# Kernel optimization log

Hardware: AMD Instinct MI355X
Metric: run time of the kernel (lower is better)

Reference implementation:

```python
import jax, jax.numpy as jnp
import numpy as np

# e2m1 FP4 positive magnitudes {0,0.5,1,1.5,2,3,4,6}/6, normalized to [0,1]
FP4_LEVELS = jnp.array([0.0, 1.0/12, 1.0/6, 1.0/4, 1.0/3, 1.0/2, 2.0/3, 1.0], dtype=jnp.float32)


def create_affp_numbers(max_val, min_val, percentile):
    # max_val, min_val: (R, G) per-group extrema -> (R, G, 16) asymmetric-float codebook
    pos = (max_val * percentile)[..., None] * FP4_LEVELS  # (R, G, 8)
    neg = (min_val * percentile)[..., None] * FP4_LEVELS  # (R, G, 8)
    return jnp.concatenate([neg, pos], axis=-1)            # (R, G, 16)


def setup_inputs() -> dict:
    key = jax.random.key(0)
    x = jax.random.normal(key, (4096, 4096), dtype=jnp.float32)
    return {"x": x, "group_size": 128, "percentile": 1}


def reference(x, group_size, percentile):
    R, C = x.shape
    G = C // group_size
    xg = x.reshape(R, G, group_size)                      # grouped view (split along dim=1)
    mx = jnp.max(xg, axis=-1)                             # (R, G)
    mn = jnp.min(xg, axis=-1)                             # (R, G)
    code = create_affp_numbers(mx, mn, jnp.float32(percentile))  # (R, G, 16)
    # full broadcast distances, argmin, gather (as in the torch source)
    dist = jnp.abs(xg[..., None] - code[:, :, None, :])   # (R, G, gs, 16)
    idx = jnp.argmin(dist, axis=-1)                       # (R, G, gs)
    q = jnp.take_along_axis(code, idx, axis=-1)           # (R, G, gs)
    return q.reshape(R, C)
```

## Files before the change

### kernel.cpp

```cpp
#include <hip/hip_runtime.h>


typedef float vfloat4 __attribute__((ext_vector_type(4)));

template <int CTRL>
__device__ __forceinline__ float dpp_mov_f32(float v) {
    return __int_as_float(__builtin_amdgcn_update_dpp(
        0, __float_as_int(v), CTRL, 0xF, 0xF, true));
}

__device__ __forceinline__ float swz_xor16_f32(float v) {
    return __int_as_float(__builtin_amdgcn_ds_swizzle(__float_as_int(v), 0x401F));
}

__global__ __launch_bounds__(256) void quant_af4_kernel(
    const float* __restrict__ x,
    const int* __restrict__ pctl_ptr,
    float* __restrict__ out,
    int n)
{
    const float LEV1 = (float)(1.0 / 12.0);
    const float LEV2 = (float)(1.0 / 6.0);
    const float LEV3 = (float)(1.0 / 4.0);
    const float LEV4 = (float)(1.0 / 3.0);
    const float LEV5 = (float)(1.0 / 2.0);
    const float LEV6 = (float)(2.0 / 3.0);
    const float LEV7 = 1.0f;

    const float percentile = (float)(*pctl_ptr);

    const int tid = blockIdx.x * blockDim.x + threadIdx.x;
    const long long base = (long long)tid * 4;
    if (base >= n) return;

    const vfloat4 v = *reinterpret_cast<const vfloat4*>(x + base);
    float vv[4] = {v.x, v.y, v.z, v.w};

    float mx = fmaxf(fmaxf(vv[0], vv[1]), fmaxf(vv[2], vv[3]));
    float mn = fminf(fminf(vv[0], vv[1]), fminf(vv[2], vv[3]));

    mx = fmaxf(mx, swz_xor16_f32(mx));
    mn = fminf(mn, swz_xor16_f32(mn));
    mx = fmaxf(mx, dpp_mov_f32<0xB1>(mx));
    mn = fminf(mn, dpp_mov_f32<0xB1>(mn));
    mx = fmaxf(mx, dpp_mov_f32<0x4E>(mx));
    mn = fminf(mn, dpp_mov_f32<0x4E>(mn));
    mx = fmaxf(mx, dpp_mov_f32<0x141>(mx));
    mn = fminf(mn, dpp_mov_f32<0x141>(mn));
    mx = fmaxf(mx, dpp_mov_f32<0x140>(mx));
    mn = fminf(mn, dpp_mov_f32<0x140>(mn));

    const float smx  = mx * percentile;
    const float smn  = mn * percentile;
    const float nabs = -smn;

    float r[4];

    if (smn <= 0.0f && smx >= 0.0f) {
        #pragma unroll
        for (int e = 0; e < 4; ++e) {
            const float xv = vv[e];
            const float a  = fabsf(xv);
            const float sp = (xv > 0.0f) ? smx : nabs;
            float dprev = a;
            float bv    = 0.0f;
            #pragma unroll
            for (int k = 1; k < 8; ++k) {
                const float L = (k == 1) ? LEV1 : (k == 2) ? LEV2 : (k == 3) ? LEV3
                              : (k == 4) ? LEV4 : (k == 5) ? LEV5 : (k == 6) ? LEV6
                              : LEV7;
                const float c = sp * L;
                const float d = a - c;
                if (fabsf(d) < fabsf(dprev)) bv = c;
                dprev = d;
            }
            const unsigned sb = __float_as_uint(xv) & 0x80000000u;
            r[e] = __uint_as_float(__float_as_uint(bv) | sb);
        }
    } else {
        float code[16];
        code[0]  = smn * 0.0f; code[1]  = smn * LEV1; code[2]  = smn * LEV2;
        code[3]  = smn * LEV3; code[4]  = smn * LEV4; code[5]  = smn * LEV5;
        code[6]  = smn * LEV6; code[7]  = smn * LEV7;
        code[8]  = smx * 0.0f; code[9]  = smx * LEV1; code[10] = smx * LEV2;
        code[11] = smx * LEV3; code[12] = smx * LEV4; code[13] = smx * LEV5;
        code[14] = smx * LEV6; code[15] = smx * LEV7;
        #pragma unroll
        for (int e = 0; e < 4; ++e) {
            const float xv = vv[e];
            float bd = fabsf(xv - code[0]);
            float bv = code[0];
            #pragma unroll
            for (int k = 1; k < 16; ++k) {
                const float d = fabsf(xv - code[k]);
                if (d < bd) { bd = d; bv = code[k]; }
            }
            r[e] = bv;
        }
    }

    vfloat4 q = {r[0], r[1], r[2], r[3]};
    __builtin_nontemporal_store(q, reinterpret_cast<vfloat4*>(out + base));
}

extern "C" void kernel_launch(void* const* d_in, const int* in_sizes, int n_in,
                              void* d_out, int out_size, void* d_ws, size_t ws_size,
                              hipStream_t stream) {
    const float* x    = (const float*)d_in[0];
    const int*   pctl = (const int*)d_in[2];
    float*       out  = (float*)d_out;

    const int n = out_size;
    const int threads = 256;
    const int elems_per_block = threads * 4;
    const int blocks = (n + elems_per_block - 1) / elems_per_block;

    quant_af4_kernel<<<blocks, threads, 0, stream>>>(x, pctl, out, n);
}
```

Baseline: 25.22 us.

## Use persistent grid-stride warps with software-prefetched next segment loads

Replaces the one-thread-per-float4 launch with a capped grid of 2048 blocks whose wavefronts loop over 256-element segments. Each wavefront loads the next segment before quantizing the current one, so memory latency overlaps with compute and block launch overhead drops. This costs extra registers for the prefetched vector and fewer resident waves. It assumes n is a multiple of 256, which holds for this group layout.

Result: slower. 27.26 us (+8.1%).

```diff
diff --git a/kernel.cpp b/kernel.cpp
--- a/kernel.cpp
+++ b/kernel.cpp
@@ -13,12 +13,7 @@
     return __int_as_float(__builtin_amdgcn_ds_swizzle(__float_as_int(v), 0x401F));
 }
 
-__global__ __launch_bounds__(256) void quant_af4_kernel(
-    const float* __restrict__ x,
-    const int* __restrict__ pctl_ptr,
-    float* __restrict__ out,
-    int n)
-{
+__device__ __forceinline__ vfloat4 quantize_seg(vfloat4 v, float percentile) {
     const float LEV1 = (float)(1.0 / 12.0);
     const float LEV2 = (float)(1.0 / 6.0);
     const float LEV3 = (float)(1.0 / 4.0);
@@ -27,18 +22,10 @@
     const float LEV6 = (float)(2.0 / 3.0);
     const float LEV7 = 1.0f;
 
-    const float percentile = (float)(*pctl_ptr);
-
-    const int tid = blockIdx.x * blockDim.x + threadIdx.x;
-    const long long base = (long long)tid * 4;
-    if (base >= n) return;
-
-    const vfloat4 v = *reinterpret_cast<const vfloat4*>(x + base);
     float vv[4] = {v.x, v.y, v.z, v.w};
 
     float mx = fmaxf(fmaxf(vv[0], vv[1]), fmaxf(vv[2], vv[3]));
     float mn = fminf(fminf(vv[0], vv[1]), fminf(vv[2], vv[3]));
-
     mx = fmaxf(mx, swz_xor16_f32(mx));
     mn = fminf(mn, swz_xor16_f32(mn));
     mx = fmaxf(mx, dpp_mov_f32<0xB1>(mx));
@@ -100,7 +87,46 @@
     }
 
     vfloat4 q = {r[0], r[1], r[2], r[3]};
-    __builtin_nontemporal_store(q, reinterpret_cast<vfloat4*>(out + base));
+    return q;
+}
+
+__global__ __launch_bounds__(256) void quant_af4_kernel(
+    const float* __restrict__ x,
+    const int* __restrict__ pctl_ptr,
+    float* __restrict__ out,
+    int n)
+{
+    const float percentile = (float)(*pctl_ptr);
+
+    const int lane = threadIdx.x & 63;
+    const int wpb  = blockDim.x >> 6;
+    const int wid  = blockIdx.x * wpb + (threadIdx.x >> 6);
+    const int nw   = gridDim.x * wpb;
+    const int nseg = n >> 8;
+
+    int seg = wid;
+    if (seg >= nseg) return;
+
+    long long base = (long long)seg * 256 + lane * 4;
+    vfloat4 v = *reinterpret_cast<const vfloat4*>(x + base);
+
+    for (;;) {
+        const int nextseg = seg + nw;
+        const bool have_next = (nextseg < nseg);
+        vfloat4 vn;
+        if (have_next) {
+            vn = *reinterpret_cast<const vfloat4*>(
+                     x + (long long)nextseg * 256 + lane * 4);
+        }
+
+        const vfloat4 q = quantize_seg(v, percentile);
+        __builtin_nontemporal_store(q, reinterpret_cast<vfloat4*>(out + base));
+
+        if (!have_next) break;
+        seg  = nextseg;
+        base = (long long)seg * 256 + lane * 4;
+        v    = vn;
+    }
 }
 
 extern "C" void kernel_launch(void* const* d_in, const int* in_sizes, int n_in,
@@ -112,8 +138,10 @@
 
     const int n = out_size;
     const int threads = 256;
-    const int elems_per_block = threads * 4;
-    const int blocks = (n + elems_per_block - 1) / elems_per_block;
+    const int nseg = n >> 8;
+    const int max_blocks = 2048;
+    const int need_blocks = (nseg + (threads >> 6) - 1) / (threads >> 6);
+    const int blocks = need_blocks < max_blocks ? need_blocks : max_blocks;
 
     quant_af4_kernel<<<blocks, threads, 0, stream>>>(x, pctl, out, n);
 }
```
